# Kernel optimization log

Hardware: AMD Instinct MI355X
Metric: run time of the kernel (lower is better)

## Reference

```python
import jax, jax.numpy as jnp
import numpy as np

B, C, H, W = 16, 256, 128, 128
C4, COUT = C // 4, 256


def setup_inputs() -> dict:
    key = jax.random.key(0)
    ks = jax.random.split(key, 8)
    s = 0.05
    flow = jax.random.normal(ks[0], (B, C, H, W), jnp.float32)
    de_out = jax.random.normal(ks[1], (B, C, H, W), jnp.float32)
    Wq = jax.random.normal(ks[2], (C4, C), jnp.float32) * s
    bq = jax.random.normal(ks[3], (C4,), jnp.float32) * s
    Wk = jax.random.normal(ks[4], (C4, C), jnp.float32) * s
    bk = jax.random.normal(ks[5], (C4,), jnp.float32) * s
    Wv = jax.random.normal(ks[6], (COUT, C), jnp.float32) * s
    bv = jax.random.normal(ks[7], (COUT,), jnp.float32) * s
    return {"flow": flow, "de_out": de_out, "Wq": Wq, "bq": bq,
            "Wk": Wk, "bk": bk, "Wv": Wv, "bv": bv}


def reference(flow, de_out, Wq, bq, Wk, bk, Wv, bv):
    # 1x1 convs == per-pixel channel matmuls
    q = jnp.einsum('bchw,dc->bdhw', de_out, Wq) + bq[None, :, None, None]  # [B,C4,H,W]
    k = jnp.einsum('bchw,dc->bdhw', flow, Wk) + bk[None, :, None, None]    # [B,C4,H,W]
    v = jnp.einsum('bchw,dc->bdhw', flow, Wv) + bv[None, :, None, None]    # [B,COUT,H,W]
    # height-axis attention per (batch, width) column
    energy = jnp.einsum('bdhw,bdgw->bwhg', q, k)          # [B,W,H,H], g = key height
    att = jax.nn.softmax(energy, axis=-1)                  # softmax over key height
    out = jnp.einsum('bcgw,bwhg->bchw', v, att)            # [B,COUT,H,W]
    return out
```

## Files before the change

### kernel.cpp

```cpp
#include <hip/hip_runtime.h>
#include <cstdint>
#include <cstddef>

typedef unsigned short u16;
using half4 = __attribute__((ext_vector_type(4))) _Float16;
using half8 = __attribute__((ext_vector_type(8))) _Float16;
using f32x4 = __attribute__((ext_vector_type(4))) float;
using f4    = __attribute__((ext_vector_type(4))) float;

#define B_    16
#define C_    256
#define H_    128
#define W_    128
#define C4_   64
#define COUT_ 256
#define HW_   (H_ * W_)

#define T_S       72
#define QK_S      72
#define P_S       136
#define XP_S      140
#define O_S       72

#define Q_ELEMS   ((size_t)B_ * W_ * H_ * C4_)
#define V_ELEMS   ((size_t)B_ * W_ * H_ * COUT_)
#define W16_ELEMS ((size_t)(C4_ * C_ + C4_ * C_ + COUT_ * C_))
#define WS_NEED   ((2 * Q_ELEMS + 2 * V_ELEMS + W16_ELEMS) * 2)

__device__ __forceinline__ u16 f16_rn(float f) {
  _Float16 h = (_Float16)f;
  return __builtin_bit_cast(u16, h);
}

__device__ __forceinline__ void gload16(const void* g, void* l) {
  __builtin_amdgcn_global_load_lds(
      (const __attribute__((address_space(1))) void*)g,
      (__attribute__((address_space(3))) void*)l, 16, 0, 0);
}

__global__ void __launch_bounds__(256) wconv_kernel(
    const float* __restrict__ Wk, const float* __restrict__ Wq,
    const float* __restrict__ Wv, u16* __restrict__ W16) {
  const int bid = blockIdx.x;
  const int t   = threadIdx.x;
  const float* src;
  u16* dst;
  int idx;
  if (bid < 16)      { src = Wk; dst = W16;                 idx = bid * 1024 + t * 4; }
  else if (bid < 32) { src = Wq; dst = W16 + C4_ * C_;      idx = (bid - 16) * 1024 + t * 4; }
  else               { src = Wv; dst = W16 + 2 * C4_ * C_;  idx = (bid - 32) * 1024 + t * 4; }
  f4 v = *reinterpret_cast<const f4*>(src + idx);
  half4 h;
#pragma unroll
  for (int i = 0; i < 4; ++i) h[i] = (_Float16)v[i];
  *reinterpret_cast<half4*>(dst + idx) = h;
}

__device__ __forceinline__ const half8* afragq(const u16* __restrict__ T,
                                               int w16, int ksl, int lg) {
  int oct = (ksl * 4 + lg) ^ ((w16 >> 2) & 7);
  return reinterpret_cast<const half8*>(&T[w16 * T_S + oct * 8]);
}

__device__ __forceinline__ const half8* whfrag(const u16* __restrict__ Wm16,
                                               int row, int ks, int lg) {
  return reinterpret_cast<const half8*>(Wm16 + (size_t)row * C_ + ks * 32 + lg * 8);
}

__global__ void __launch_bounds__(256, 3) qkv_kernel(
    const float* __restrict__ flow, const float* __restrict__ de_out,
    const u16* __restrict__ W16,
    const float* __restrict__ bq, const float* __restrict__ bk,
    const float* __restrict__ bv,
    u16* __restrict__ Qws, u16* __restrict__ Kws, u16* __restrict__ Vws) {
  __shared__ __align__(16) unsigned char ldsraw[2 * 16384 + 64 * T_S * 2];
  float* Fbuf[2] = {reinterpret_cast<float*>(ldsraw),
                    reinterpret_cast<float*>(ldsraw + 16384)};
  u16* T = reinterpret_cast<u16*>(ldsraw + 32768);
  u16* O = reinterpret_cast<u16*>(ldsraw);

  const int t    = threadIdx.x;
  const int bid  = blockIdx.x;
  const int g      = (bid & 7) | ((bid >> 6) << 3);
  const int hlow   = (bid >> 3) & 7;
  const int w0     = (g & 1) * 64;
  const int hgrp   = (g >> 1) & 15;
  const int b      = (g >> 5) & 15;
  const int srcsel = g >> 9;
  const int h      = hgrp * 8 + hlow;
  const int lane = t & 63;
  const int wv   = t >> 6;
  const int col  = lane & 15;
  const int lg   = lane >> 4;

  const u16* Wk16 = W16;
  const u16* Wq16 = W16 + C4_ * C_;
  const u16* Wv16 = W16 + 2 * C4_ * C_;

  const float* src =
      (srcsel ? de_out : flow) + (size_t)b * C_ * HW_ + (size_t)h * W_ + w0;

  f32x4 zero = {0.f, 0.f, 0.f, 0.f};
  f32x4 acc0[4];
  f32x4 accV[4][4];
#pragma unroll
  for (int i = 0; i < 4; ++i) acc0[i] = zero;
#pragma unroll
  for (int j = 0; j < 4; ++j)
#pragma unroll
    for (int i = 0; i < 4; ++i) accV[j][i] = zero;

#pragma unroll
  for (int i = 0; i < 4; ++i) {
    const int rr0 = wv * 16 + i * 4;
    gload16(src + (size_t)(rr0 + (lane >> 4)) * HW_ + (lane & 15) * 4,
            Fbuf[0] + rr0 * 64);
  }

#pragma unroll
  for (int q = 0; q < 4; ++q) {
    float* Fc = Fbuf[q & 1];
    float* Fn = Fbuf[(q + 1) & 1];
    if (q < 3) {
      const float* s = src + (size_t)((q + 1) * 64) * HW_;
#pragma unroll
      for (int i = 0; i < 4; ++i) {
        const int rr0 = wv * 16 + i * 4;
        gload16(s + (size_t)(rr0 + (lane >> 4)) * HW_ + (lane & 15) * 4,
                Fn + rr0 * 64);
      }
      asm volatile("s_waitcnt vmcnt(4) lgkmcnt(0)\ns_barrier" ::: "memory");
    } else {
      asm volatile("s_waitcnt vmcnt(0) lgkmcnt(0)\ns_barrier" ::: "memory");
    }
    __builtin_amdgcn_sched_barrier(0);

#pragma unroll
    for (int i = 0; i < 2; ++i) {
      const int flat = i * 256 + t;
      const int wq = flat & 15;
      const int pp = flat >> 4;
      const f4 fa = *reinterpret_cast<const f4*>(&Fc[(2 * pp) * 64 + wq * 4]);
      const f4 fb = *reinterpret_cast<const f4*>(&Fc[(2 * pp + 1) * 64 + wq * 4]);
      const int c_loc = 2 * pp;
      const int oct   = (c_loc >> 3) ^ (wq & 7);
#pragma unroll
      for (int j = 0; j < 4; ++j) {
        const int w = wq * 4 + j;
        uint32_t pk = (uint32_t)f16_rn(fa[j]) | ((uint32_t)f16_rn(fb[j]) << 16);
        *reinterpret_cast<uint32_t*>(&T[w * T_S + oct * 8 + (c_loc & 7)]) = pk;
      }
    }
    asm volatile("s_waitcnt lgkmcnt(0)\ns_barrier" ::: "memory");
    __builtin_amdgcn_sched_barrier(0);

#pragma unroll
    for (int ksl = 0; ksl < 2; ++ksl) {
      const int ks = 2 * q + ksl;
      if (srcsel == 0) {
        const half8 bK = *whfrag(Wk16, wv * 16 + col, ks, lg);
        half8 bV[4];
#pragma unroll
        for (int j = 0; j < 4; ++j)
          bV[j] = *whfrag(Wv16, (wv * 4 + j) * 16 + col, ks, lg);
#pragma unroll
        for (int wt = 0; wt < 4; ++wt) {
          const half8 afr = *afragq(T, wt * 16 + col, ksl, lg);
          acc0[wt] = __builtin_amdgcn_mfma_f32_16x16x32_f16(afr, bK, acc0[wt], 0, 0, 0);
#pragma unroll
          for (int j = 0; j < 4; ++j)
            accV[j][wt] =
                __builtin_amdgcn_mfma_f32_16x16x32_f16(afr, bV[j], accV[j][wt], 0, 0, 0);
        }
      } else {
        const half8 bQ = *whfrag(Wq16, wv * 16 + col, ks, lg);
#pragma unroll
        for (int wt = 0; wt < 4; ++wt) {
          const half8 afr = *afragq(T, wt * 16 + col, ksl, lg);
          acc0[wt] = __builtin_amdgcn_mfma_f32_16x16x32_f16(afr, bQ, acc0[wt], 0, 0, 0);
        }
      }
    }
  }

  if (srcsel == 0) {
    {
      const float bias = bk[wv * 16 + col];
      __syncthreads();
#pragma unroll
      for (int wt = 0; wt < 4; ++wt)
#pragma unroll
        for (int r = 0; r < 4; ++r)
          O[(wt * 16 + lg * 4 + r) * O_S + wv * 16 + col] = f16_rn(acc0[wt][r] + bias);
      __syncthreads();
#pragma unroll
      for (int i = 0; i < 2; ++i) {
        const int item = i * 256 + t;
        const int wl = item >> 3;
        const int d0 = (item & 7) * 8;
        *reinterpret_cast<half8*>(
            &Kws[(((size_t)b * W_ + w0 + wl) * H_ + h) * C4_ + d0]) =
            *reinterpret_cast<const half8*>(&O[wl * O_S + d0]);
      }
    }
#pragma unroll
    for (int j = 0; j < 4; ++j) {
      const int co = (wv * 4 + j) * 16 + col;
      const float bias = bv[co];
#pragma unroll
      for (int wt = 0; wt < 4; ++wt)
#pragma unroll
        for (int r = 0; r < 4; ++r) {
          int w = w0 + wt * 16 + lg * 4 + r;
          Vws[(size_t)(b * W_ + w) * 32768 + ((h >> 3) * COUT_ + co) * 8 + (h & 7)] =
              f16_rn(accV[j][wt][r] + bias);
        }
    }
  } else {
    const float bias = bq[wv * 16 + col];
    __syncthreads();
#pragma unroll
    for (int wt = 0; wt < 4; ++wt)
#pragma unroll
      for (int r = 0; r < 4; ++r)
        O[(wt * 16 + lg * 4 + r) * O_S + wv * 16 + col] = f16_rn(acc0[wt][r] + bias);
    __syncthreads();
#pragma unroll
    for (int i = 0; i < 2; ++i) {
      const int item = i * 256 + t;
      const int wl = item >> 3;
      const int d0 = (item & 7) * 8;
      *reinterpret_cast<half8*>(
          &Qws[(((size_t)b * W_ + w0 + wl) * H_ + h) * C4_ + d0]) =
          *reinterpret_cast<const half8*>(&O[wl * O_S + d0]);
    }
  }
}

template <int EPI>
__global__ void __launch_bounds__(512, 4) attn_kernel(
    const u16* __restrict__ Qws, const u16* __restrict__ Kws,
    const u16* __restrict__ Vws, u16* __restrict__ out_tmp,
    float* __restrict__ out) {
  __shared__ __align__(16) u16 ldsQK[2 * 128 * QK_S];

  const int t   = threadIdx.x;
  const int bid = blockIdx.x;
  const int sw  = (bid & 7) * 256 + (bid >> 3);
  const int b   = sw >> 7;
  const int w   = sw & 127;
  const int lane = t & 63;
  const int wv   = t >> 6;
  const int col  = lane & 15;
  const int lg   = lane >> 4;

  const u16* qc    = Qws + ((size_t)b * W_ + w) * H_ * C4_;
  const u16* kc    = Kws + ((size_t)b * W_ + w) * H_ * C4_;
  const u16* vbase = Vws + (size_t)(b * W_ + w) * 32768;

  u16* ldsQ = ldsQK;
  u16* ldsK = ldsQK + 128 * QK_S;

#pragma unroll
  for (int i = 0; i < 2; ++i) {
    int item = i * 512 + t;
    int hh   = item >> 3;
    int d0   = (item & 7) * 8;
    *reinterpret_cast<half8*>(&ldsQ[hh * QK_S + d0]) =
        *reinterpret_cast<const half8*>(qc + item * 8);
    *reinterpret_cast<half8*>(&ldsK[hh * QK_S + d0]) =
        *reinterpret_cast<const half8*>(kc + item * 8);
  }
  __syncthreads();

  f32x4 zero = {0.f, 0.f, 0.f, 0.f};

  f32x4 e[8];
#pragma unroll
  for (int gt = 0; gt < 8; ++gt) e[gt] = zero;
#pragma unroll
  for (int ks = 0; ks < 2; ++ks) {
    const half8 aq = *reinterpret_cast<const half8*>(
        &ldsQ[(wv * 16 + col) * QK_S + ks * 32 + lg * 8]);
#pragma unroll
    for (int gt = 0; gt < 8; ++gt) {
      const half8 bkf = *reinterpret_cast<const half8*>(
          &ldsK[(gt * 16 + col) * QK_S + ks * 32 + lg * 8]);
      e[gt] = __builtin_amdgcn_mfma_f32_16x16x32_f16(aq, bkf, e[gt], 0, 0, 0);
    }
  }
  __syncthreads();

  u16* ldsP = ldsQK;

#pragma unroll
  for (int r = 0; r < 4; ++r) {
    float m = -1e30f;
#pragma unroll
    for (int gt = 0; gt < 8; ++gt) m = fmaxf(m, e[gt][r]);
#pragma unroll
    for (int off = 1; off < 16; off <<= 1) m = fmaxf(m, __shfl_xor(m, off));
    float s = 0.f;
#pragma unroll
    for (int gt = 0; gt < 8; ++gt) {
      float p = __expf(e[gt][r] - m);
      e[gt][r] = p;
      s += p;
    }
#pragma unroll
    for (int off = 1; off < 16; off <<= 1) s += __shfl_xor(s, off);
    const float inv = 1.f / s;
    const int hh = wv * 16 + lg * 4 + r;
#pragma unroll
    for (int gt = 0; gt < 8; ++gt)
      ldsP[hh * P_S + gt * 16 + col] = f16_rn(e[gt][r] * inv);
  }

  f32x4 o[16];
#pragma unroll
  for (int ct = 0; ct < 16; ++ct) o[ct] = zero;
#pragma unroll
  for (int ks = 0; ks < 4; ++ks) {
    const half8 ap = *reinterpret_cast<const half8*>(
        &ldsP[(wv * 16 + col) * P_S + ks * 32 + lg * 8]);
#pragma unroll
    for (int ct = 0; ct < 16; ++ct) {
      const half8 bvf = *reinterpret_cast<const half8*>(
          vbase + ((ks * 4 + lg) * COUT_ + ct * 16 + col) * 8);
      o[ct] = __builtin_amdgcn_mfma_f32_16x16x32_f16(ap, bvf, o[ct], 0, 0, 0);
    }
  }

  if (EPI == 1) {
    u16* ldsX = ldsQK;
    u16* dst_col = out_tmp + ((size_t)(b * W_ + w) << 15);
#pragma unroll
    for (int ctg = 0; ctg < 4; ++ctg) {
      __syncthreads();
#pragma unroll
      for (int j = 0; j < 4; ++j) {
        const int ct    = ctg * 4 + j;
        const int c_loc = j * 16 + col;
        half4 pk;
#pragma unroll
        for (int r = 0; r < 4; ++r) pk[r] = (_Float16)o[ct][r];
        *reinterpret_cast<half4*>(&ldsX[c_loc * XP_S + wv * 16 + lg * 4]) = pk;
      }
      __syncthreads();
      const int c_loc = t >> 3;
      const int h0    = (t & 7) * 16;
      u16* dp = dst_col + (ctg * 64 + c_loc) * 128 + h0;
      *reinterpret_cast<half8*>(dp) =
          *reinterpret_cast<const half8*>(&ldsX[c_loc * XP_S + h0]);
      *reinterpret_cast<half8*>(dp + 8) =
          *reinterpret_cast<const half8*>(&ldsX[c_loc * XP_S + h0 + 8]);
    }
  } else {
    float* outp = out + (size_t)b * COUT_ * HW_ + w;
#pragma unroll
    for (int ct = 0; ct < 16; ++ct)
#pragma unroll
      for (int r = 0; r < 4; ++r) {
        int hrow = wv * 16 + lg * 4 + r;
        int c = ct * 16 + col;
        outp[((size_t)c * H_ + hrow) * W_] = o[ct][r];
      }
  }
}

__global__ void __launch_bounds__(256) transpose_kernel(
    const u16* __restrict__ T, float* __restrict__ out) {
  __shared__ float lds[64 * 132];
  const int t   = threadIdx.x;
  const int bid = blockIdx.x;
  const int b   = bid >> 9;
  const int ft  = bid & 511;

  {
    const int w  = t >> 1;
    const int fo = (t & 1) * 32;
    const u16* src = T + ((size_t)(b * W_ + w) << 15) + ft * 64 + fo;
#pragma unroll
    for (int k = 0; k < 4; ++k) {
      half8 v = *reinterpret_cast<const half8*>(src + k * 8);
#pragma unroll
      for (int e = 0; e < 8; ++e)
        lds[(fo + k * 8 + e) * 132 + w] = (float)v[e];
    }
  }
  __syncthreads();
  {
    const int f_loc = t >> 2;
    const int w0    = (t & 3) * 32;
    float* dst = out + (size_t)b * (COUT_ * HW_) + (size_t)(ft * 64 + f_loc) * 128 + w0;
#pragma unroll
    for (int k = 0; k < 8; ++k) {
      f4 v4;
#pragma unroll
      for (int e = 0; e < 4; ++e) v4[e] = lds[f_loc * 132 + w0 + k * 4 + e];
      *reinterpret_cast<f4*>(dst + k * 4) = v4;
    }
  }
}

extern "C" void kernel_launch(void* const* d_in, const int* in_sizes, int n_in,
                              void* d_out, int out_size, void* d_ws, size_t ws_size,
                              hipStream_t stream) {
  const float* flow   = (const float*)d_in[0];
  const float* de_out = (const float*)d_in[1];
  const float* Wq = (const float*)d_in[2];
  const float* bq = (const float*)d_in[3];
  const float* Wk = (const float*)d_in[4];
  const float* bk = (const float*)d_in[5];
  const float* Wv = (const float*)d_in[6];
  const float* bv = (const float*)d_in[7];
  float* out = (float*)d_out;

  u16* Qws = (u16*)d_ws;
  u16* Kws = Qws + Q_ELEMS;
  u16* Vws = Kws + Q_ELEMS;
  u16* W16 = Vws + V_ELEMS;
  u16* Tws = W16 + W16_ELEMS;

  wconv_kernel<<<96, 256, 0, stream>>>(Wk, Wq, Wv, W16);
  qkv_kernel<<<2 * B_ * H_ * 2, 256, 0, stream>>>(flow, de_out, W16, bq, bk, bv,
                                                  Qws, Kws, Vws);
  if (ws_size >= (size_t)WS_NEED) {
    attn_kernel<1><<<B_ * W_, 512, 0, stream>>>(Qws, Kws, Vws, Tws, out);
    transpose_kernel<<<B_ * 512, 256, 0, stream>>>(Tws, out);
  } else {
    attn_kernel<0><<<B_ * W_, 512, 0, stream>>>(Qws, Kws, Vws, Tws, out);
  }
}
```

Baseline: 445.9 us.

## Widen QKV projection blocks to full 128-wide rows and drop double buffering

The QKV projection kernel now runs 512-thread blocks that each cover a full 128-pixel row instead of two 64-pixel halves, halving the grid. Work is split so each wave owns 16 pixels and loops over all output channel tiles, loading weight fragments from global per MFMA rather than holding them in registers. The double-buffered async prefetch of input channel chunks is replaced by a single buffer with a full wait each iteration. This aims to reuse each weight fetch across more pixels and cut block count, at the cost of losing load/compute overlap and using more accumulator registers (16 V tiles per wave).

```diff
diff --git a/kernel.cpp b/kernel.cpp
--- a/kernel.cpp
+++ b/kernel.cpp
@@ -57,9 +57,9 @@
 }
 
 __device__ __forceinline__ const half8* afragq(const u16* __restrict__ T,
-                                               int w16, int ksl, int lg) {
-  int oct = (ksl * 4 + lg) ^ ((w16 >> 2) & 7);
-  return reinterpret_cast<const half8*>(&T[w16 * T_S + oct * 8]);
+                                               int prow, int ksl, int lg) {
+  int oct = (ksl * 4 + lg) ^ ((prow >> 2) & 7);
+  return reinterpret_cast<const half8*>(&T[prow * T_S + oct * 8]);
 }
 
 __device__ __forceinline__ const half8* whfrag(const u16* __restrict__ Wm16,
@@ -67,26 +67,24 @@
   return reinterpret_cast<const half8*>(Wm16 + (size_t)row * C_ + ks * 32 + lg * 8);
 }
 
-__global__ void __launch_bounds__(256, 3) qkv_kernel(
+__global__ void __launch_bounds__(512, 4) qkv_kernel(
     const float* __restrict__ flow, const float* __restrict__ de_out,
     const u16* __restrict__ W16,
     const float* __restrict__ bq, const float* __restrict__ bk,
     const float* __restrict__ bv,
     u16* __restrict__ Qws, u16* __restrict__ Kws, u16* __restrict__ Vws) {
-  __shared__ __align__(16) unsigned char ldsraw[2 * 16384 + 64 * T_S * 2];
-  float* Fbuf[2] = {reinterpret_cast<float*>(ldsraw),
-                    reinterpret_cast<float*>(ldsraw + 16384)};
-  u16* T = reinterpret_cast<u16*>(ldsraw + 32768);
-  u16* O = reinterpret_cast<u16*>(ldsraw);
+  __shared__ __align__(16) unsigned char ldsraw[32768 + 128 * T_S * 2];
+  float* F = reinterpret_cast<float*>(ldsraw);
+  u16*   T = reinterpret_cast<u16*>(ldsraw + 32768);
+  u16*   O = reinterpret_cast<u16*>(ldsraw);
 
   const int t    = threadIdx.x;
   const int bid  = blockIdx.x;
-  const int g      = (bid & 7) | ((bid >> 6) << 3);
+  const int g2     = (bid & 7) | ((bid >> 6) << 3);
   const int hlow   = (bid >> 3) & 7;
-  const int w0     = (g & 1) * 64;
-  const int hgrp   = (g >> 1) & 15;
-  const int b      = (g >> 5) & 15;
-  const int srcsel = g >> 9;
+  const int hgrp   = g2 & 15;
+  const int srcsel = (g2 >> 4) & 1;
+  const int b      = g2 >> 5;
   const int h      = hgrp * 8 + hlow;
   const int lane = t & 63;
   const int wv   = t >> 6;
@@ -98,50 +96,33 @@
   const u16* Wv16 = W16 + 2 * C4_ * C_;
 
   const float* src =
-      (srcsel ? de_out : flow) + (size_t)b * C_ * HW_ + (size_t)h * W_ + w0;
+      (srcsel ? de_out : flow) + (size_t)b * C_ * HW_ + (size_t)h * W_;
 
   f32x4 zero = {0.f, 0.f, 0.f, 0.f};
   f32x4 acc0[4];
-  f32x4 accV[4][4];
+  f32x4 accV[16];
 #pragma unroll
   for (int i = 0; i < 4; ++i) acc0[i] = zero;
 #pragma unroll
-  for (int j = 0; j < 4; ++j)
-#pragma unroll
-    for (int i = 0; i < 4; ++i) accV[j][i] = zero;
-
-#pragma unroll
-  for (int i = 0; i < 4; ++i) {
-    const int rr0 = wv * 16 + i * 4;
-    gload16(src + (size_t)(rr0 + (lane >> 4)) * HW_ + (lane & 15) * 4,
-            Fbuf[0] + rr0 * 64);
-  }
-
-#pragma unroll
+  for (int i = 0; i < 16; ++i) accV[i] = zero;
+
   for (int q = 0; q < 4; ++q) {
-    float* Fc = Fbuf[q & 1];
-    float* Fn = Fbuf[(q + 1) & 1];
-    if (q < 3) {
-      const float* s = src + (size_t)((q + 1) * 64) * HW_;
-#pragma unroll
-      for (int i = 0; i < 4; ++i) {
-        const int rr0 = wv * 16 + i * 4;
-        gload16(s + (size_t)(rr0 + (lane >> 4)) * HW_ + (lane & 15) * 4,
-                Fn + rr0 * 64);
-      }
-      asm volatile("s_waitcnt vmcnt(4) lgkmcnt(0)\ns_barrier" ::: "memory");
-    } else {
-      asm volatile("s_waitcnt vmcnt(0) lgkmcnt(0)\ns_barrier" ::: "memory");
-    }
+#pragma unroll
+    for (int i = 0; i < 4; ++i) {
+      const int r0 = wv * 8 + i * 2;
+      gload16(src + (size_t)(q * 64 + r0 + (lane >> 5)) * HW_ + (lane & 31) * 4,
+              F + r0 * 128);
+    }
+    asm volatile("s_waitcnt vmcnt(0) lgkmcnt(0)\ns_barrier" ::: "memory");
     __builtin_amdgcn_sched_barrier(0);
 
 #pragma unroll
     for (int i = 0; i < 2; ++i) {
-      const int flat = i * 256 + t;
-      const int wq = flat & 15;
-      const int pp = flat >> 4;
-      const f4 fa = *reinterpret_cast<const f4*>(&Fc[(2 * pp) * 64 + wq * 4]);
-      const f4 fb = *reinterpret_cast<const f4*>(&Fc[(2 * pp + 1) * 64 + wq * 4]);
+      const int flat = i * 512 + t;
+      const int wq = flat & 31;
+      const int pp = flat >> 5;
+      const f4 fa = *reinterpret_cast<const f4*>(&F[(2 * pp) * 128 + wq * 4]);
+      const f4 fb = *reinterpret_cast<const f4*>(&F[(2 * pp + 1) * 128 + wq * 4]);
       const int c_loc = 2 * pp;
       const int oct   = (c_loc >> 3) ^ (wq & 7);
 #pragma unroll
@@ -157,82 +138,61 @@
 #pragma unroll
     for (int ksl = 0; ksl < 2; ++ksl) {
       const int ks = 2 * q + ksl;
+      const half8 afr = *afragq(T, wv * 16 + col, ksl, lg);
       if (srcsel == 0) {
-        const half8 bK = *whfrag(Wk16, wv * 16 + col, ks, lg);
-        half8 bV[4];
-#pragma unroll
-        for (int j = 0; j < 4; ++j)
-          bV[j] = *whfrag(Wv16, (wv * 4 + j) * 16 + col, ks, lg);
-#pragma unroll
-        for (int wt = 0; wt < 4; ++wt) {
-          const half8 afr = *afragq(T, wt * 16 + col, ksl, lg);
-          acc0[wt] = __builtin_amdgcn_mfma_f32_16x16x32_f16(afr, bK, acc0[wt], 0, 0, 0);
-#pragma unroll
-          for (int j = 0; j < 4; ++j)
-            accV[j][wt] =
-                __builtin_amdgcn_mfma_f32_16x16x32_f16(afr, bV[j], accV[j][wt], 0, 0, 0);
-        }
+#pragma unroll
+        for (int nt = 0; nt < 4; ++nt)
+          acc0[nt] = __builtin_amdgcn_mfma_f32_16x16x32_f16(
+              afr, *whfrag(Wk16, nt * 16 + col, ks, lg), acc0[nt], 0, 0, 0);
+#pragma unroll
+        for (int j = 0; j < 16; ++j)
+          accV[j] = __builtin_amdgcn_mfma_f32_16x16x32_f16(
+              afr, *whfrag(Wv16, j * 16 + col, ks, lg), accV[j], 0, 0, 0);
       } else {
-        const half8 bQ = *whfrag(Wq16, wv * 16 + col, ks, lg);
-#pragma unroll
-        for (int wt = 0; wt < 4; ++wt) {
-          const half8 afr = *afragq(T, wt * 16 + col, ksl, lg);
-          acc0[wt] = __builtin_amdgcn_mfma_f32_16x16x32_f16(afr, bQ, acc0[wt], 0, 0, 0);
-        }
-      }
-    }
-  }
-
-  if (srcsel == 0) {
-    {
-      const float bias = bk[wv * 16 + col];
-      __syncthreads();
-#pragma unroll
-      for (int wt = 0; wt < 4; ++wt)
-#pragma unroll
-        for (int r = 0; r < 4; ++r)
-          O[(wt * 16 + lg * 4 + r) * O_S + wv * 16 + col] = f16_rn(acc0[wt][r] + bias);
-      __syncthreads();
-#pragma unroll
-      for (int i = 0; i < 2; ++i) {
-        const int item = i * 256 + t;
-        const int wl = item >> 3;
-        const int d0 = (item & 7) * 8;
-        *reinterpret_cast<half8*>(
-            &Kws[(((size_t)b * W_ + w0 + wl) * H_ + h) * C4_ + d0]) =
-            *reinterpret_cast<const half8*>(&O[wl * O_S + d0]);
-      }
-    }
-#pragma unroll
-    for (int j = 0; j < 4; ++j) {
-      const int co = (wv * 4 + j) * 16 + col;
-      const float bias = bv[co];
-#pragma unroll
-      for (int wt = 0; wt < 4; ++wt)
-#pragma unroll
-        for (int r = 0; r < 4; ++r) {
-          int w = w0 + wt * 16 + lg * 4 + r;
-          Vws[(size_t)(b * W_ + w) * 32768 + ((h >> 3) * COUT_ + co) * 8 + (h & 7)] =
-              f16_rn(accV[j][wt][r] + bias);
-        }
-    }
-  } else {
-    const float bias = bq[wv * 16 + col];
+#pragma unroll
+        for (int nt = 0; nt < 4; ++nt)
+          acc0[nt] = __builtin_amdgcn_mfma_f32_16x16x32_f16(
+              afr, *whfrag(Wq16, nt * 16 + col, ks, lg), acc0[nt], 0, 0, 0);
+      }
+    }
+  }
+
+  {
+    const float* bias_v = (srcsel == 0) ? bk : bq;
+    const float bias = bias_v[0 * 16 + 0], dummy = bias;
+    (void)dummy;
     __syncthreads();
 #pragma unroll
-    for (int wt = 0; wt < 4; ++wt)
+    for (int nt = 0; nt < 4; ++nt) {
+      const float bs = bias_v[nt * 16 + col];
 #pragma unroll
       for (int r = 0; r < 4; ++r)
-        O[(wt * 16 + lg * 4 + r) * O_S + wv * 16 + col] = f16_rn(acc0[wt][r] + bias);
+        O[(wv * 16 + lg * 4 + r) * O_S + nt * 16 + col] = f16_rn(acc0[nt][r] + bs);
+    }
     __syncthreads();
+    u16* dstKQ = (srcsel == 0) ? Kws : Qws;
 #pragma unroll
     for (int i = 0; i < 2; ++i) {
-      const int item = i * 256 + t;
+      const int item = i * 512 + t;
       const int wl = item >> 3;
       const int d0 = (item & 7) * 8;
       *reinterpret_cast<half8*>(
-          &Qws[(((size_t)b * W_ + w0 + wl) * H_ + h) * C4_ + d0]) =
+          &dstKQ[(((size_t)b * W_ + wl) * H_ + h) * C4_ + d0]) =
           *reinterpret_cast<const half8*>(&O[wl * O_S + d0]);
+    }
+  }
+
+  if (srcsel == 0) {
+#pragma unroll
+    for (int j = 0; j < 16; ++j) {
+      const int co = j * 16 + col;
+      const float bias = bv[co];
+#pragma unroll
+      for (int r = 0; r < 4; ++r) {
+        const int w = wv * 16 + lg * 4 + r;
+        Vws[(size_t)(b * W_ + w) * 32768 + ((h >> 3) * COUT_ + co) * 8 + (h & 7)] =
+            f16_rn(accV[j][r] + bias);
+      }
     }
   }
 }
@@ -423,8 +383,8 @@
   u16* Tws = W16 + W16_ELEMS;
 
   wconv_kernel<<<96, 256, 0, stream>>>(Wk, Wq, Wv, W16);
-  qkv_kernel<<<2 * B_ * H_ * 2, 256, 0, stream>>>(flow, de_out, W16, bq, bk, bv,
-                                                  Qws, Kws, Vws);
+  qkv_kernel<<<2 * B_ * H_, 512, 0, stream>>>(flow, de_out, W16, bq, bk, bv,
+                                              Qws, Kws, Vws);
   if (ws_size >= (size_t)WS_NEED) {
     attn_kernel<1><<<B_ * W_, 512, 0, stream>>>(Qws, Kws, Vws, Tws, out);
     transpose_kernel<<<B_ * 512, 256, 0, stream>>>(Tws, out);
```

Result: slower. 693.1 us (+55.4%).
